# Performance work log

Measured on AMD Instinct MI355X. Metric: run time of the kernel, lower is better.

## Reference

```python
import jax, jax.numpy as jnp
import numpy as np

N_NODES = 100000
N_EDGES = 3200000
NUM_GRAPHS = 512
D_IN, D_H = 7, 16


def gcn_conv(x, edge_index, W, b, n_nodes):
    # PyG GCNConv: x' = D^{-1/2} (A + I) D^{-1/2} X W + b
    h = x @ W  # [N, d_out] -- do the tiny GEMM first (fewer bytes moved per edge)
    row, col = edge_index[0], edge_index[1]  # messages flow row -> col
    loop = jnp.arange(n_nodes)
    row = jnp.concatenate([row, loop])
    col = jnp.concatenate([col, loop])
    deg = jax.ops.segment_sum(jnp.ones(row.shape[0], dtype=h.dtype), col,
                              num_segments=n_nodes)
    dinv = jnp.where(deg > 0, jax.lax.rsqrt(deg), 0.0)
    norm = dinv[row] * dinv[col]                      # [E+N]
    msg = h[row] * norm[:, None]                      # gather + scale
    out = jax.ops.segment_sum(msg, col, num_segments=n_nodes)  # scatter-add
    return out + b


def setup_inputs() -> dict:
    key = jax.random.key(0)
    ks = jax.random.split(key, 9)
    x = jax.random.normal(ks[0], (N_NODES, D_IN), dtype=jnp.float32)
    edge_index = jax.random.randint(ks[1], (2, N_EDGES), 0, N_NODES, dtype=jnp.int64)
    batch = jnp.sort(jax.random.randint(ks[2], (N_NODES,), 0, NUM_GRAPHS, dtype=jnp.int64))
    def glorot(k, fan_in, fan_out):
        lim = np.sqrt(6.0 / (fan_in + fan_out)).astype(np.float32)
        return jax.random.uniform(k, (fan_in, fan_out), jnp.float32, -lim, lim)
    return {
        "x": x, "edge_index": edge_index, "batch": batch,
        "W1": glorot(ks[3], D_IN, D_H), "b1": jnp.zeros((D_H,), jnp.float32),
        "W2": glorot(ks[4], D_H, D_H), "b2": jnp.zeros((D_H,), jnp.float32),
        "Wl": glorot(ks[5], D_H, 1),   "bl": jnp.zeros((1,), jnp.float32),
    }


def reference(x, edge_index, batch, W1, b1, W2, b2, Wl, bl):
    n = x.shape[0]
    h = jax.nn.relu(gcn_conv(x, edge_index, W1, b1, n))
    h = jax.nn.relu(gcn_conv(h, edge_index, W2, b2, n))
    # global_mean_pool over graphs
    sums = jax.ops.segment_sum(h, batch, num_segments=NUM_GRAPHS)
    cnts = jax.ops.segment_sum(jnp.ones((n,), h.dtype), batch, num_segments=NUM_GRAPHS)
    pooled = sums / jnp.maximum(cnts, 1.0)[:, None]   # [G, 16]
    out = jax.nn.sigmoid(pooled @ Wl + bl)            # [G, 1]
    return out.squeeze(1)                             # [G]
```

## Files before the change

kernel.cpp:

```cpp
#include <hip/hip_runtime.h>
#include <hip/hip_fp16.h>
#include <math.h>

#define N_NODES    100000
#define N_EDGES    3200000
#define NUM_GRAPHS 512
#define D_IN       7
#define D_H        16
#define D_H2       8
#define SHIFT      7
#define BWIDTH     128
#define NB         782
#define CHUNK      4096
#define NCH        782
#define PC         4
#define PB         2
#define TPH        36
#define HST        (8 * TPH)

__global__ void hist_kernel(const int* __restrict__ col, int* __restrict__ cnt) {
    __shared__ int lh[NB];
    int tid = threadIdx.x;
    for (int i = tid; i < NB; i += blockDim.x) lh[i] = 0;
    __syncthreads();
    int e0 = blockIdx.x * CHUNK;
    int e1 = e0 + CHUNK; if (e1 > N_EDGES) e1 = N_EDGES;
    for (int e = e0 + tid; e < e1; e += blockDim.x)
        atomicAdd(&lh[col[e] >> SHIFT], 1);
    __syncthreads();
    int* outp = cnt + (size_t)blockIdx.x * NB;
    for (int i = tid; i < NB; i += blockDim.x) outp[i] = lh[i];
}

__global__ void colscan_kernel(const int* __restrict__ cnt, int* __restrict__ base,
                               int* __restrict__ bcnt) {
    __shared__ int ts[256];
    int b = blockIdx.x;
    int tid = threadIdx.x;
    int c0 = tid * PC;
    int vals[PC];
    int sum = 0;
#pragma unroll
    for (int q = 0; q < PC; ++q) {
        int c = c0 + q;
        int v = (c < NCH) ? cnt[(size_t)c * NB + b] : 0;
        vals[q] = v; sum += v;
    }
    ts[tid] = sum;
    __syncthreads();
    for (int st = 1; st < 256; st <<= 1) {
        int v = (tid >= st) ? ts[tid - st] : 0;
        __syncthreads();
        ts[tid] += v;
        __syncthreads();
    }
    int run = ts[tid] - sum;
    int* bp = base + (size_t)b * NCH;
#pragma unroll
    for (int q = 0; q < PC; ++q) {
        int c = c0 + q;
        if (c < NCH) { bp[c] = run; run += vals[q]; }
    }
    if (tid == 0) bcnt[b] = ts[255];
}

__global__ void scan_kernel(const int* __restrict__ bcnt, int* __restrict__ offs) {
    __shared__ int lds[1024];
    int tid = threadIdx.x;
    lds[tid] = (tid < NB) ? bcnt[tid] : 0;
    __syncthreads();
    for (int st = 1; st < 1024; st <<= 1) {
        int v = (tid >= st) ? lds[tid - st] : 0;
        __syncthreads();
        lds[tid] += v;
        __syncthreads();
    }
    if (tid < NB) offs[tid + 1] = lds[tid];
    if (tid == 0) offs[0] = 0;
}

__global__ void place_kernel(const int* __restrict__ row, const int* __restrict__ col,
                             const int* __restrict__ base, const int* __restrict__ offs,
                             int* __restrict__ part) {
    __shared__ int lh[NB];
    __shared__ int sc[NB];
    __shared__ int lb[NB];
    __shared__ int ts[512];
    __shared__ int stage[CHUNK];
    __shared__ int dstv[CHUNK];

    int c = blockIdx.x;
    int tid = threadIdx.x;
    int e0 = c * CHUNK;
    int e1 = e0 + CHUNK; if (e1 > N_EDGES) e1 = N_EDGES;
    int n  = e1 - e0;

    for (int i = tid; i < NB; i += blockDim.x) lh[i] = 0;
    __syncthreads();
    for (int e = e0 + tid; e < e1; e += blockDim.x)
        atomicAdd(&lh[col[e] >> SHIFT], 1);
    __syncthreads();
    int b0 = tid * PB;
    int vals[PB];
    int sum = 0;
#pragma unroll
    for (int q = 0; q < PB; ++q) {
        int b = b0 + q;
        int v = (b < NB) ? lh[b] : 0;
        vals[q] = v; sum += v;
    }
    ts[tid] = sum;
    __syncthreads();
    for (int st = 1; st < 512; st <<= 1) {
        int v = (tid >= st) ? ts[tid - st] : 0;
        __syncthreads();
        ts[tid] += v;
        __syncthreads();
    }
    int run = ts[tid] - sum;
#pragma unroll
    for (int q = 0; q < PB; ++q) {
        int b = b0 + q;
        if (b < NB) {
            sc[b] = run;
            lb[b] = offs[b] + base[(size_t)b * NCH + c];
            run += vals[q];
            lh[b] = 0;
        }
    }
    __syncthreads();
    for (int e = e0 + tid; e < e1; e += blockDim.x) {
        int cc = col[e];
        int b = cc >> SHIFT;
        int rank = atomicAdd(&lh[b], 1);
        int loc = sc[b] + rank;
        stage[loc] = (row[e] << SHIFT) | (cc & (BWIDTH - 1));
        dstv[loc]  = lb[b] + rank;
    }
    __syncthreads();
    for (int i = tid; i < n; i += blockDim.x)
        part[dstv[i]] = stage[i];
}

__global__ void csr_kernel(const int* __restrict__ part, const int* __restrict__ offs,
                           int* __restrict__ csr, int* __restrict__ node_off,
                           int* __restrict__ deg, float* __restrict__ dinv) {
    __shared__ int cnt[BWIDTH];
    __shared__ int scn[BWIDTH];
    __shared__ int cur[BWIDTH];
    int b = blockIdx.x;
    int o0 = offs[b], o1 = offs[b + 1];
    if (threadIdx.x < BWIDTH) cnt[threadIdx.x] = 0;
    __syncthreads();
    for (int j = o0 + threadIdx.x; j < o1; j += blockDim.x)
        atomicAdd(&cnt[part[j] & (BWIDTH - 1)], 1);
    __syncthreads();
    if (threadIdx.x < BWIDTH) scn[threadIdx.x] = cnt[threadIdx.x];
    __syncthreads();
    for (int st = 1; st < BWIDTH; st <<= 1) {
        int v = 0;
        if (threadIdx.x < BWIDTH && threadIdx.x >= st) v = scn[threadIdx.x - st];
        __syncthreads();
        if (threadIdx.x < BWIDTH) scn[threadIdx.x] += v;
        __syncthreads();
    }
    if (threadIdx.x < BWIDTH) {
        int excl = scn[threadIdx.x] - cnt[threadIdx.x];
        cur[threadIdx.x] = excl;
        int c = b * BWIDTH + threadIdx.x;
        if (c < N_NODES) {
            node_off[c] = o0 + excl;
            deg[c] = cnt[threadIdx.x];
            dinv[c] = rsqrtf((float)cnt[threadIdx.x] + 1.0f);
        }
    }
    __syncthreads();
    for (int j = o0 + threadIdx.x; j < o1; j += blockDim.x) {
        int e = part[j];
        int l = e & (BWIDTH - 1);
        int pos = atomicAdd(&cur[l], 1);
        csr[o0 + pos] = e >> SHIFT;
    }
}

__global__ void xw1_kernel(const float* __restrict__ x, const float* __restrict__ W1,
                           const float* __restrict__ dinv, unsigned* __restrict__ sh) {
    int v = blockIdx.x * blockDim.x + threadIdx.x;
    if (v >= N_NODES) return;
    float xv[D_IN];
#pragma unroll
    for (int j = 0; j < D_IN; ++j) xv[j] = x[v * D_IN + j];
    float dv = dinv[v];
#pragma unroll
    for (int k2 = 0; k2 < D_H2; ++k2) {
        float a0 = 0.f, a1 = 0.f;
#pragma unroll
        for (int j = 0; j < D_IN; ++j) {
            a0 += xv[j] * W1[j * D_H + 2 * k2];
            a1 += xv[j] * W1[j * D_H + 2 * k2 + 1];
        }
        __half2 p = __floats2half2_rn(a0 * dv, a1 * dv);
        sh[v * D_H2 + k2] = *(unsigned*)&p;
    }
}

__device__ __forceinline__ float gather_half(const unsigned* __restrict__ sh,
                                             const int* __restrict__ csr,
                                             int o0, int d, unsigned* stg, int l) {
    int g = l >> 4, k = l & 15;
    const uint4* rp = (const uint4*)(stg + (k >> 1) * TPH + g * 16);
    bool hi = (k & 1);
    float acc = 0.f;
    for (int base = 0; base < d; base += 32) {
        int j = base + l;
        uint4 a = make_uint4(0u, 0u, 0u, 0u), b = make_uint4(0u, 0u, 0u, 0u);
        if (j < d) {
            int r = __builtin_nontemporal_load(&csr[o0 + j]);
            const uint4* sp = (const uint4*)(sh + (size_t)r * D_H2);
            a = sp[0];
            b = sp[1];
        }
        asm volatile("s_waitcnt lgkmcnt(0)" ::: "memory");
        stg[0 * TPH + l] = a.x;
        stg[1 * TPH + l] = a.y;
        stg[2 * TPH + l] = a.z;
        stg[3 * TPH + l] = a.w;
        stg[4 * TPH + l] = b.x;
        stg[5 * TPH + l] = b.y;
        stg[6 * TPH + l] = b.z;
        stg[7 * TPH + l] = b.w;
        asm volatile("s_waitcnt lgkmcnt(0)" ::: "memory");
        uint4 q0 = rp[0], q1 = rp[1], q2 = rp[2], q3 = rp[3];
        unsigned ws[16] = { q0.x, q0.y, q0.z, q0.w, q1.x, q1.y, q1.z, q1.w,
                            q2.x, q2.y, q2.z, q2.w, q3.x, q3.y, q3.z, q3.w };
#pragma unroll
        for (int i = 0; i < 16; ++i) {
            __half2 p = *(__half2*)&ws[i];
            acc += hi ? __high2float(p) : __low2float(p);
        }
    }
    acc += __shfl_xor(acc, 16, 64);
    return acc;
}

__global__ void __launch_bounds__(256, 8)
pull1_kernel(const unsigned* __restrict__ sh, const int* __restrict__ csr,
             const int* __restrict__ node_off, const int* __restrict__ deg,
             const float* __restrict__ dinv, const float* __restrict__ b1,
             const float* __restrict__ W2, unsigned* __restrict__ s2h) {
    __shared__ unsigned stage[4][2 * HST];
    __shared__ float hrow[4][2][D_H];
    int wave = threadIdx.x >> 6;
    int lane = threadIdx.x & 63;
    int h = lane >> 5, l = lane & 31;
    int v = blockIdx.x * 8 + wave * 2 + h;
    int k = l & 15;
    float w2c[D_H];
#pragma unroll
    for (int j = 0; j < D_H; ++j) w2c[j] = W2[j * D_H + k];
    int d = deg[v], o0 = node_off[v];
    unsigned* stg = stage[wave] + h * HST;
    float acc = gather_half(sh, csr, o0, d, stg, l);
    float dv = dinv[v];
    if (l < 16) {
        unsigned ws = sh[(size_t)v * D_H2 + (k >> 1)];
        __half2 ps = *(__half2*)&ws;
        float selfv = (k & 1) ? __high2float(ps) : __low2float(ps);
        float hv = fmaxf(dv * (acc + selfv) + b1[k], 0.f);
        hrow[wave][h][k] = hv;
    }
    asm volatile("s_waitcnt lgkmcnt(0)" ::: "memory");
    const float4* hp = (const float4*)hrow[wave][h];
    float4 h0 = hp[0], h1 = hp[1], h2 = hp[2], h3 = hp[3];
    float a2 = h0.x * w2c[0] + h0.y * w2c[1] + h0.z * w2c[2] + h0.w * w2c[3]
             + h1.x * w2c[4] + h1.y * w2c[5] + h1.z * w2c[6] + h1.w * w2c[7]
             + h2.x * w2c[8] + h2.y * w2c[9] + h2.z * w2c[10] + h2.w * w2c[11]
             + h3.x * w2c[12] + h3.y * w2c[13] + h3.z * w2c[14] + h3.w * w2c[15];
    a2 *= dv;
    float a2hi = __shfl_xor(a2, 1, 64);
    if (l < 16 && (k & 1) == 0) {
        __half2 p = __floats2half2_rn(a2, a2hi);
        s2h[(size_t)v * D_H2 + (k >> 1)] = *(unsigned*)&p;
    }
}

__global__ void __launch_bounds__(256, 8)
pull2_kernel(const unsigned* __restrict__ sh, const int* __restrict__ csr,
             const int* __restrict__ node_off, const int* __restrict__ deg,
             const float* __restrict__ dinv, const float* __restrict__ b2,
             float* __restrict__ h2) {
    __shared__ unsigned stage[4][2 * HST];
    int wave = threadIdx.x >> 6;
    int lane = threadIdx.x & 63;
    int h = lane >> 5, l = lane & 31;
    int v = blockIdx.x * 8 + wave * 2 + h;
    int k = l & 15;
    int d = deg[v], o0 = node_off[v];
    unsigned* stg = stage[wave] + h * HST;
    float acc = gather_half(sh, csr, o0, d, stg, l);
    if (l < 16) {
        float dv = dinv[v];
        unsigned ws = sh[(size_t)v * D_H2 + (k >> 1)];
        __half2 ps = *(__half2*)&ws;
        float selfv = (k & 1) ? __high2float(ps) : __low2float(ps);
        float o = dv * (acc + selfv) + b2[k];
        h2[(size_t)v * D_H + k] = fmaxf(o, 0.f);
    }
}

__global__ void starts_kernel(const int* __restrict__ batch, int* __restrict__ starts) {
    int v = blockIdx.x * blockDim.x + threadIdx.x;
    if (v >= N_NODES) return;
    int bv = batch[v];
    int prev = (v == 0) ? -1 : batch[v - 1];
    for (int g = prev + 1; g <= bv; ++g) starts[g] = v;
    if (v == N_NODES - 1) {
        for (int g = bv + 1; g <= NUM_GRAPHS; ++g) starts[g] = N_NODES;
    }
}

__global__ void pool_head_kernel(const float* __restrict__ h, const int* __restrict__ starts,
                                 const float* __restrict__ Wl, const float* __restrict__ bl,
                                 float* __restrict__ out) {
    int g = blockIdx.x;
    int v0 = starts[g], v1 = starts[g + 1];
    int k = threadIdx.x & 15;
    int vi = threadIdx.x >> 4;
    float acc = 0.f;
    for (int v = v0 + vi; v < v1; v += 16) acc += h[v * D_H + k];
    acc += __shfl_xor(acc, 16, 64);
    acc += __shfl_xor(acc, 32, 64);
    __shared__ float sm[4][D_H];
    int lane = threadIdx.x & 63;
    if (lane < 16) sm[threadIdx.x >> 6][k] = acc;
    __syncthreads();
    if (threadIdx.x < 16) {
        float tot = sm[0][k] + sm[1][k] + sm[2][k] + sm[3][k];
        float cntf = (float)(v1 - v0);
        tot /= fmaxf(cntf, 1.0f);
        float p = tot * Wl[k];
        p += __shfl_xor(p, 1, 64);
        p += __shfl_xor(p, 2, 64);
        p += __shfl_xor(p, 4, 64);
        p += __shfl_xor(p, 8, 64);
        if (k == 0) out[g] = 1.0f / (1.0f + expf(-(p + bl[0])));
    }
}


extern "C" void kernel_launch(void* const* d_in, const int* in_sizes, int n_in,
                              void* d_out, int out_size, void* d_ws, size_t ws_size,
                              hipStream_t stream) {
    const float* x     = (const float*)d_in[0];
    const int*   ei    = (const int*)d_in[1];
    const int*   batch = (const int*)d_in[2];
    const float* W1    = (const float*)d_in[3];
    const float* b1    = (const float*)d_in[4];
    const float* W2    = (const float*)d_in[5];
    const float* b2    = (const float*)d_in[6];
    const float* Wl    = (const float*)d_in[7];
    const float* bl    = (const float*)d_in[8];
    float* out = (float*)d_out;

    const int* row = ei;
    const int* col = ei + N_EDGES;

    char* wsb = (char*)d_ws;
    size_t o = 0;
    int*      part     = (int*)(wsb + o);      o += (size_t)N_EDGES * 4;
    char*     regionA  = wsb + o;              o += (size_t)N_EDGES * 4;
    int*      cnt      = (int*)regionA;
    int*      base     = (int*)(regionA + (size_t)NCH * NB * 4);
    int*      csr      = (int*)regionA;
    int*      bcnt     = (int*)(wsb + o);      o += 1024 * 4;
    int*      offs     = (int*)(wsb + o);      o += 1024 * 4;
    int*      node_off = (int*)(wsb + o);      o += 100352 * 4;
    int*      deg      = (int*)(wsb + o);      o += 100352 * 4;
    float*    dinv     = (float*)(wsb + o);    o += 100352 * 4;
    unsigned* sAh      = (unsigned*)(wsb + o); o += (size_t)N_NODES * D_H2 * 4;
    unsigned* sBh      = (unsigned*)(wsb + o); o += (size_t)N_NODES * D_H2 * 4;
    float*    h2       = (float*)(wsb + o);    o += (size_t)N_NODES * D_H * 4;
    int*      starts   = (int*)(wsb + o);      o += 1024 * 4;

    const int B = 256;
    const int NVB = (N_NODES + B - 1) / B;

    hist_kernel<<<NCH, 512, 0, stream>>>(col, cnt);
    colscan_kernel<<<NB, B, 0, stream>>>(cnt, base, bcnt);
    scan_kernel<<<1, 1024, 0, stream>>>(bcnt, offs);
    place_kernel<<<NCH, 512, 0, stream>>>(row, col, base, offs, part);
    csr_kernel<<<NB, 512, 0, stream>>>(part, offs, csr, node_off, deg, dinv);

    xw1_kernel<<<NVB, B, 0, stream>>>(x, W1, dinv, sAh);
    pull1_kernel<<<N_NODES / 8, B, 0, stream>>>(sAh, csr, node_off, deg, dinv,
                                                b1, W2, sBh);
    pull2_kernel<<<N_NODES / 8, B, 0, stream>>>(sBh, csr, node_off, deg, dinv,
                                                b2, h2);
    starts_kernel<<<NVB, B, 0, stream>>>(batch, starts);
    pool_head_kernel<<<NUM_GRAPHS, B, 0, stream>>>(h2, starts, Wl, bl, out);
}
```

Before: 144.9 us.

## Aggregate raw scaled features before W1 in layer one, halving gather bytes

Layer one now gathers dinv-scaled 7-wide input features (packed as 8 halves, 16 bytes per row) instead of the precomputed 16-wide X·W1 rows (32 bytes). The W1 multiply is applied after aggregation inside pull1, which lowers per-edge gather traffic and LDS staging work. The edge-binning chunk size is also doubled, halving the hist/place block count. The cost is extra per-node math in pull1 and different half-precision rounding, since x is quantised before the W1 product.

```diff
diff --git a/kernel.cpp b/kernel.cpp
--- a/kernel.cpp
+++ b/kernel.cpp
@@ -11,12 +11,14 @@
 #define SHIFT      7
 #define BWIDTH     128
 #define NB         782
-#define CHUNK      4096
-#define NCH        782
-#define PC         4
+#define CHUNK      8192
+#define NCH        391
+#define PC         2
 #define PB         2
 #define TPH        36
 #define HST        (8 * TPH)
+#define TP1        36
+#define HST1       (4 * TP1)
 
 __global__ void hist_kernel(const int* __restrict__ col, int* __restrict__ cnt) {
     __shared__ int lh[NB];
@@ -183,24 +185,99 @@
     }
 }
 
-__global__ void xw1_kernel(const float* __restrict__ x, const float* __restrict__ W1,
-                           const float* __restrict__ dinv, unsigned* __restrict__ sh) {
+__global__ void xs_kernel(const float* __restrict__ x, const float* __restrict__ dinv,
+                          unsigned* __restrict__ xsh) {
     int v = blockIdx.x * blockDim.x + threadIdx.x;
     if (v >= N_NODES) return;
-    float xv[D_IN];
-#pragma unroll
-    for (int j = 0; j < D_IN; ++j) xv[j] = x[v * D_IN + j];
     float dv = dinv[v];
-#pragma unroll
-    for (int k2 = 0; k2 < D_H2; ++k2) {
-        float a0 = 0.f, a1 = 0.f;
-#pragma unroll
-        for (int j = 0; j < D_IN; ++j) {
-            a0 += xv[j] * W1[j * D_H + 2 * k2];
-            a1 += xv[j] * W1[j * D_H + 2 * k2 + 1];
-        }
-        __half2 p = __floats2half2_rn(a0 * dv, a1 * dv);
-        sh[v * D_H2 + k2] = *(unsigned*)&p;
+    float xv[8];
+#pragma unroll
+    for (int j = 0; j < D_IN; ++j) xv[j] = x[v * D_IN + j] * dv;
+    xv[7] = 0.f;
+#pragma unroll
+    for (int w = 0; w < 4; ++w) {
+        __half2 p = __floats2half2_rn(xv[2 * w], xv[2 * w + 1]);
+        xsh[(size_t)v * 4 + w] = *(unsigned*)&p;
+    }
+}
+
+__global__ void __launch_bounds__(256, 8)
+pull1_kernel(const unsigned* __restrict__ xsh, const int* __restrict__ csr,
+             const int* __restrict__ node_off, const int* __restrict__ deg,
+             const float* __restrict__ dinv, const float* __restrict__ b1,
+             const float* __restrict__ W1, const float* __restrict__ W2,
+             unsigned* __restrict__ s2h) {
+    __shared__ unsigned stage[4][2 * HST1];
+    __shared__ float aggrow[4][2][8];
+    __shared__ float hrow[4][2][D_H];
+    int wave = threadIdx.x >> 6;
+    int lane = threadIdx.x & 63;
+    int h = lane >> 5, l = lane & 31;
+    int v = blockIdx.x * 8 + wave * 2 + h;
+    int k = l & 15;
+    float w1c[D_IN];
+#pragma unroll
+    for (int j = 0; j < D_IN; ++j) w1c[j] = W1[j * D_H + k];
+    float w2c[D_H];
+#pragma unroll
+    for (int j = 0; j < D_H; ++j) w2c[j] = W2[j * D_H + k];
+    int d = deg[v], o0 = node_off[v];
+    unsigned* stg = stage[wave] + h * HST1;
+    int rg = l >> 3, p = l & 7;
+    int w = p >> 1;
+    bool hi = (p & 1);
+    const uint4* rp = (const uint4*)(stg + w * TP1 + rg * 8);
+    float acc = 0.f;
+    for (int base = 0; base < d; base += 32) {
+        int j = base + l;
+        uint4 a = make_uint4(0u, 0u, 0u, 0u);
+        if (j < d) {
+            int r = __builtin_nontemporal_load(&csr[o0 + j]);
+            a = *(const uint4*)(xsh + (size_t)r * 4);
+        }
+        asm volatile("s_waitcnt lgkmcnt(0)" ::: "memory");
+        stg[0 * TP1 + l] = a.x;
+        stg[1 * TP1 + l] = a.y;
+        stg[2 * TP1 + l] = a.z;
+        stg[3 * TP1 + l] = a.w;
+        asm volatile("s_waitcnt lgkmcnt(0)" ::: "memory");
+        uint4 q0 = rp[0], q1 = rp[1];
+        unsigned ws[8] = { q0.x, q0.y, q0.z, q0.w, q1.x, q1.y, q1.z, q1.w };
+#pragma unroll
+        for (int i = 0; i < 8; ++i) {
+            __half2 ph = *(__half2*)&ws[i];
+            acc += hi ? __high2float(ph) : __low2float(ph);
+        }
+    }
+    acc += __shfl_xor(acc, 8, 64);
+    acc += __shfl_xor(acc, 16, 64);
+    float dv = dinv[v];
+    if (l < 8) aggrow[wave][h][l] = acc;
+    asm volatile("s_waitcnt lgkmcnt(0)" ::: "memory");
+    uint4 sx = *(const uint4*)(xsh + (size_t)v * 4);
+    unsigned sxw[4] = { sx.x, sx.y, sx.z, sx.w };
+    const float* ag = aggrow[wave][h];
+    float hv = b1[k];
+#pragma unroll
+    for (int j = 0; j < D_IN; ++j) {
+        __half2 ph = *(__half2*)&sxw[j >> 1];
+        float xsv = (j & 1) ? __high2float(ph) : __low2float(ph);
+        hv += dv * (ag[j] + xsv) * w1c[j];
+    }
+    hv = fmaxf(hv, 0.f);
+    if (l < 16) hrow[wave][h][k] = hv;
+    asm volatile("s_waitcnt lgkmcnt(0)" ::: "memory");
+    const float4* hp = (const float4*)hrow[wave][h];
+    float4 h0 = hp[0], h1 = hp[1], h2 = hp[2], h3 = hp[3];
+    float a2 = h0.x * w2c[0] + h0.y * w2c[1] + h0.z * w2c[2] + h0.w * w2c[3]
+             + h1.x * w2c[4] + h1.y * w2c[5] + h1.z * w2c[6] + h1.w * w2c[7]
+             + h2.x * w2c[8] + h2.y * w2c[9] + h2.z * w2c[10] + h2.w * w2c[11]
+             + h3.x * w2c[12] + h3.y * w2c[13] + h3.z * w2c[14] + h3.w * w2c[15];
+    a2 *= dv;
+    float a2hi = __shfl_xor(a2, 1, 64);
+    if (l < 16 && (k & 1) == 0) {
+        __half2 pq = __floats2half2_rn(a2, a2hi);
+        s2h[(size_t)v * D_H2 + (k >> 1)] = *(unsigned*)&pq;
     }
 }
 
@@ -241,47 +318,6 @@
     }
     acc += __shfl_xor(acc, 16, 64);
     return acc;
-}
-
-__global__ void __launch_bounds__(256, 8)
-pull1_kernel(const unsigned* __restrict__ sh, const int* __restrict__ csr,
-             const int* __restrict__ node_off, const int* __restrict__ deg,
-             const float* __restrict__ dinv, const float* __restrict__ b1,
-             const float* __restrict__ W2, unsigned* __restrict__ s2h) {
-    __shared__ unsigned stage[4][2 * HST];
-    __shared__ float hrow[4][2][D_H];
-    int wave = threadIdx.x >> 6;
-    int lane = threadIdx.x & 63;
-    int h = lane >> 5, l = lane & 31;
-    int v = blockIdx.x * 8 + wave * 2 + h;
-    int k = l & 15;
-    float w2c[D_H];
-#pragma unroll
-    for (int j = 0; j < D_H; ++j) w2c[j] = W2[j * D_H + k];
-    int d = deg[v], o0 = node_off[v];
-    unsigned* stg = stage[wave] + h * HST;
-    float acc = gather_half(sh, csr, o0, d, stg, l);
-    float dv = dinv[v];
-    if (l < 16) {
-        unsigned ws = sh[(size_t)v * D_H2 + (k >> 1)];
-        __half2 ps = *(__half2*)&ws;
-        float selfv = (k & 1) ? __high2float(ps) : __low2float(ps);
-        float hv = fmaxf(dv * (acc + selfv) + b1[k], 0.f);
-        hrow[wave][h][k] = hv;
-    }
-    asm volatile("s_waitcnt lgkmcnt(0)" ::: "memory");
-    const float4* hp = (const float4*)hrow[wave][h];
-    float4 h0 = hp[0], h1 = hp[1], h2 = hp[2], h3 = hp[3];
-    float a2 = h0.x * w2c[0] + h0.y * w2c[1] + h0.z * w2c[2] + h0.w * w2c[3]
-             + h1.x * w2c[4] + h1.y * w2c[5] + h1.z * w2c[6] + h1.w * w2c[7]
-             + h2.x * w2c[8] + h2.y * w2c[9] + h2.z * w2c[10] + h2.w * w2c[11]
-             + h3.x * w2c[12] + h3.y * w2c[13] + h3.z * w2c[14] + h3.w * w2c[15];
-    a2 *= dv;
-    float a2hi = __shfl_xor(a2, 1, 64);
-    if (l < 16 && (k & 1) == 0) {
-        __half2 p = __floats2half2_rn(a2, a2hi);
-        s2h[(size_t)v * D_H2 + (k >> 1)] = *(unsigned*)&p;
-    }
 }
 
 __global__ void __launch_bounds__(256, 8)
@@ -377,7 +413,7 @@
     int*      node_off = (int*)(wsb + o);      o += 100352 * 4;
     int*      deg      = (int*)(wsb + o);      o += 100352 * 4;
     float*    dinv     = (float*)(wsb + o);    o += 100352 * 4;
-    unsigned* sAh      = (unsigned*)(wsb + o); o += (size_t)N_NODES * D_H2 * 4;
+    unsigned* xsh      = (unsigned*)(wsb + o); o += (size_t)N_NODES * 4 * 4;
     unsigned* sBh      = (unsigned*)(wsb + o); o += (size_t)N_NODES * D_H2 * 4;
     float*    h2       = (float*)(wsb + o);    o += (size_t)N_NODES * D_H * 4;
     int*      starts   = (int*)(wsb + o);      o += 1024 * 4;
@@ -391,9 +427,9 @@
     place_kernel<<<NCH, 512, 0, stream>>>(row, col, base, offs, part);
     csr_kernel<<<NB, 512, 0, stream>>>(part, offs, csr, node_off, deg, dinv);
 
-    xw1_kernel<<<NVB, B, 0, stream>>>(x, W1, dinv, sAh);
-    pull1_kernel<<<N_NODES / 8, B, 0, stream>>>(sAh, csr, node_off, deg, dinv,
-                                                b1, W2, sBh);
+    xs_kernel<<<NVB, B, 0, stream>>>(x, dinv, xsh);
+    pull1_kernel<<<N_NODES / 8, B, 0, stream>>>(xsh, csr, node_off, deg, dinv,
+                                                b1, W1, W2, sBh);
     pull2_kernel<<<N_NODES / 8, B, 0, stream>>>(sBh, csr, node_off, deg, dinv,
                                                 b2, h2);
     starts_kernel<<<NVB, B, 0, stream>>>(batch, starts);
```

After: 131.8 us (median of 2 runs). -9.0%, faster.
